# Kernel tuning notes

Hardware: AMD Instinct MI355X
Metric: run time of the kernel (lower is better)

Reference implementation:

```python
import jax, jax.numpy as jnp
import numpy as np

B, S, D, H, E, K = 4, 2048, 1024, 4096, 8, 2
CAP = 2048      # expert capacity (tokens)
ALPHA = 0.01    # load-balance loss coefficient


def setup_inputs() -> dict:
    key = jax.random.key(0)
    ks = jax.random.split(key, 8)
    def w(k, shape, fan_in):
        return jax.random.normal(k, shape, jnp.float32) * (fan_in ** -0.5)
    return {
        "input": jax.random.normal(ks[0], (B, S, D), jnp.float32),
        "rw": w(ks[1], (D, E), D), "rb": jnp.zeros((E,), jnp.float32),
        "w1": w(ks[2], (E, D, H), D), "b1": jnp.zeros((E, H), jnp.float32),
        "w2": w(ks[3], (E, H, D), H), "b2": jnp.zeros((E, D), jnp.float32),
        "ow1": w(ks[4], (D, H), D), "ob1": jnp.zeros((H,), jnp.float32),
        "ow2": w(ks[5], (H, D), H), "ob2": jnp.zeros((D,), jnp.float32),
    }


def _moe(x, rw, rb, w1, b1, w2, b2, ow1, ob1, ow2, ob2):
    Bx, Sx, Dx = x.shape
    N = Bx * Sx
    xf = x.reshape(N, Dx)

    # --- router: softmax -> top-k -> renormalize ---
    scores = jax.nn.softmax(xf @ rw + rb, axis=-1)          # [N,E]
    tw, ti = jax.lax.top_k(scores, K)                       # [N,K]
    tw = tw / tw.sum(-1, keepdims=True)
    onehot = jax.nn.one_hot(ti, E, dtype=xf.dtype)          # [N,K,E]
    w_ne = jnp.einsum('nk,nke->ne', tw, onehot)             # combine weight per (token, expert)
    mask = onehot.sum(1) > 0                                # [N,E]
    mi = mask.astype(jnp.int32)

    # exclusive rank of each token within its expert's queue (token order, as torch nonzero())
    rank = jnp.cumsum(mi, axis=0) - mi                      # [N,E]
    within = mask & (rank < CAP)
    over = mask & (rank >= CAP)

    # --- dispatch within-capacity tokens into [E, CAP] slots (sentinel = N) ---
    tok = jnp.broadcast_to(jnp.arange(N, dtype=jnp.int32)[:, None], (N, E))
    eid = jnp.broadcast_to(jnp.arange(E, dtype=jnp.int32)[None, :], (N, E))
    slot = jnp.where(within, rank, CAP)                     # non-assigned -> pad column
    buf = jnp.full((E, CAP + 1), N, dtype=jnp.int32)
    buf = buf.at[eid.reshape(-1), slot.reshape(-1)].set(tok.reshape(-1))
    buf = buf[:, :CAP]                                      # [E,CAP]

    xpad = jnp.concatenate([xf, jnp.zeros((1, Dx), xf.dtype)], axis=0)
    xd = xpad[buf]                                          # [E,CAP,D]

    # --- grouped expert FFN (Linear -> relu -> Linear) ---
    h = jax.nn.relu(jnp.einsum('ecd,edh->ech', xd, w1) + b1[:, None, :])
    y = jnp.einsum('ech,ehd->ecd', h, w2) + b2[:, None, :]  # [E,CAP,D]

    # combine weights gathered per slot; pad slots get weight 0
    wpad = jnp.concatenate([w_ne, jnp.zeros((1, E), w_ne.dtype)], axis=0)
    wc = wpad[buf, jnp.arange(E, dtype=jnp.int32)[:, None]]  # [E,CAP]

    outpad = jnp.zeros((N + 1, Dx), xf.dtype)
    outpad = outpad.at[buf.reshape(-1)].add((wc[..., None] * y).reshape(-1, Dx))
    out = outpad[:N]

    # --- overflow tokens -> shared overflow FFN (computed densely, masked by weight) ---
    w_of = (w_ne * over.astype(w_ne.dtype)).sum(-1)          # [N]
    yo = jax.nn.relu(xf @ ow1 + ob1) @ ow2 + ob2             # [N,D]
    out = out + w_of[:, None] * yo

    # --- aux load-balance loss (detached in torch via .item()) ---
    num = mi.sum(0)                                          # [E]
    cnt = jnp.minimum(num, CAP)
    f = cnt.astype(xf.dtype) / N
    p = (w_ne * within.astype(w_ne.dtype)).sum(0) / jnp.maximum(cnt, 1).astype(xf.dtype)
    aux = ALPHA * E * jnp.sum(f * p)
    return out.reshape(Bx, Sx, Dx), jax.lax.stop_gradient(aux)


def reference(input, rw, rb, w1, b1, w2, b2, ow1, ob1, ow2, ob2):
    return _moe(input, rw, rb, w1, b1, w2, b2, ow1, ob1, ow2, ob2)
```

## Files before the change

kernel.cpp:

```cpp
#include <hip/hip_runtime.h>
#include <cstdint>

typedef __attribute__((ext_vector_type(8))) short bf16x8;
typedef __attribute__((ext_vector_type(4))) float f32x4;

#define N_TOK    8192
#define DMODEL   1024
#define HDIM     4096
#define CAPACITY 2048

__device__ __forceinline__ unsigned short f2bf(float f) {
  unsigned u = __float_as_uint(f);
  u += 0x7FFFu + ((u >> 16) & 1u);
  return (unsigned short)(u >> 16);
}

__device__ __forceinline__ void gl_lds16(const unsigned short* g, unsigned short* l) {
  __builtin_amdgcn_global_load_lds(
      (const __attribute__((address_space(1))) void*)g,
      (__attribute__((address_space(3))) void*)l, 16, 0, 0);
}

__global__ void cvtx_kernel(const float* __restrict__ x, unsigned short* __restrict__ xb) {
  long i0 = ((long)blockIdx.x * 256 + threadIdx.x) * 16;
#pragma unroll
  for (int ii = 0; ii < 4; ii++) {
    float4 v = *(const float4*)(x + i0 + ii * 4);
    ushort4 u;
    u.x = f2bf(v.x); u.y = f2bf(v.y); u.z = f2bf(v.z); u.w = f2bf(v.w);
    *(ushort4*)(xb + i0 + ii * 4) = u;
  }
}

__global__ void router_kernel(const float* __restrict__ x, const float* __restrict__ rw,
                              const float* __restrict__ rb, int4* __restrict__ recs) {
  int wave = threadIdx.x >> 6;
  int lane = threadIdx.x & 63;
  int tok = blockIdx.x * 4 + wave;
  const float* xr = x + (long)tok * DMODEL;
  float s[8];
#pragma unroll
  for (int e = 0; e < 8; e++) s[e] = 0.f;
  for (int ii = 0; ii < DMODEL / 64; ii++) {
    int k = lane + 64 * ii;
    float xv = xr[k];
    const float* wr = rw + k * 8;
    float4 a = *(const float4*)wr;
    float4 b = *(const float4*)(wr + 4);
    s[0] += xv * a.x; s[1] += xv * a.y; s[2] += xv * a.z; s[3] += xv * a.w;
    s[4] += xv * b.x; s[5] += xv * b.y; s[6] += xv * b.z; s[7] += xv * b.w;
  }
#pragma unroll
  for (int m = 1; m < 64; m <<= 1) {
#pragma unroll
    for (int e = 0; e < 8; e++) s[e] += __shfl_xor(s[e], m);
  }
  if (lane == 0) {
#pragma unroll
    for (int e = 0; e < 8; e++) s[e] += rb[e];
    int b0 = 0; float v0 = s[0];
#pragma unroll
    for (int e = 1; e < 8; e++) if (s[e] > v0) { v0 = s[e]; b0 = e; }
    int b1 = -1; float v1 = 0.f;
#pragma unroll
    for (int e = 0; e < 8; e++) {
      if (e == b0) continue;
      if (b1 < 0 || s[e] > v1) { v1 = s[e]; b1 = e; }
    }
    float t0 = 1.f / (1.f + expf(v1 - v0));
    float t1 = 1.f - t0;
    recs[tok] = make_int4(b0, b1, __float_as_int(t0), __float_as_int(t1));
  }
}

__device__ __forceinline__ int bump16(uint4& v, int e) {
  unsigned sh = (e & 1) ? 16u : 0u;
  unsigned inc = 1u << sh;
  unsigned old;
  switch (e >> 1) {
    case 0: old = v.x; v.x += inc; break;
    case 1: old = v.y; v.y += inc; break;
    case 2: old = v.z; v.z += inc; break;
    default: old = v.w; v.w += inc; break;
  }
  return (int)((old >> sh) & 0xFFFFu);
}

__device__ __forceinline__ unsigned field16(uint4 v, int e) {
  unsigned w;
  switch (e >> 1) { case 0: w = v.x; break; case 1: w = v.y; break; case 2: w = v.z; break; default: w = v.w; break; }
  return (w >> ((e & 1) ? 16 : 0)) & 0xFFFFu;
}

__global__ void assign_kernel(const int4* __restrict__ recs, int* __restrict__ buf,
                              float* __restrict__ wc, int* __restrict__ cnt,
                              float* __restrict__ auxOut) {
  __shared__ uint4 sc[1024];
  __shared__ unsigned sco[1024];
  __shared__ float pnum[8];
  int tid = threadIdx.x;
  if (tid < 8) pnum[tid] = 0.f;
  int4 rc[8];
#pragma unroll
  for (int i = 0; i < 8; i++) {
    rc[i] = recs[tid * 8 + i];
    rc[i].x &= 7; rc[i].y &= 7;
  }
  uint4 c; c.x = c.y = c.z = c.w = 0u;
#pragma unroll
  for (int i = 0; i < 8; i++) { bump16(c, rc[i].x); bump16(c, rc[i].y); }
  sc[tid] = c;
  __syncthreads();
  for (int off = 1; off < 1024; off <<= 1) {
    uint4 v; v.x = v.y = v.z = v.w = 0u;
    if (tid >= off) v = sc[tid - off];
    __syncthreads();
    sc[tid].x += v.x; sc[tid].y += v.y; sc[tid].z += v.z; sc[tid].w += v.w;
    __syncthreads();
  }
  uint4 base; base.x = base.y = base.z = base.w = 0u;
  if (tid > 0) base = sc[tid - 1];
  uint4 totals = sc[1023];

  uint4 run = base;
  float wof[8];
  unsigned oc = 0;
#pragma unroll
  for (int i = 0; i < 8; i++) {
    int tk = tid * 8 + i;
    int e0 = rc[i].x, e1 = rc[i].y;
    float w0 = __int_as_float(rc[i].z);
    float w1 = __int_as_float(rc[i].w);
    float w = 0.f;
    int r0 = bump16(run, e0);
    if (r0 < CAPACITY) {
      buf[e0 * CAPACITY + r0] = tk;
      wc[e0 * CAPACITY + r0] = w0;
      atomicAdd(&pnum[e0], w0);
    } else w += w0;
    int r1 = bump16(run, e1);
    if (r1 < CAPACITY) {
      buf[e1 * CAPACITY + r1] = tk;
      wc[e1 * CAPACITY + r1] = w1;
      atomicAdd(&pnum[e1], w1);
    } else w += w1;
    wof[i] = w;
    if (w > 0.f) oc++;
  }
  sco[tid] = oc;
  __syncthreads();
  for (int off = 1; off < 1024; off <<= 1) {
    unsigned v = (tid >= off) ? sco[tid - off] : 0u;
    __syncthreads();
    sco[tid] += v;
    __syncthreads();
  }
  unsigned ob = (tid > 0) ? sco[tid - 1] : 0u;
  unsigned Ot = sco[1023];
#pragma unroll
  for (int i = 0; i < 8; i++) {
    if (wof[i] > 0.f) {
      unsigned slot = ob++;
      int ve = 8 + (int)(slot >> 11);
      buf[ve * CAPACITY + (int)(slot & 2047)] = tid * 8 + i;
      wc[ve * CAPACITY + (int)(slot & 2047)] = wof[i];
    }
  }
  __syncthreads();
  if (tid == 0) {
    float aux = 0.f;
#pragma unroll
    for (int e = 0; e < 8; e++) {
      int tot = (int)field16(totals, e);
      int c2 = tot < CAPACITY ? tot : CAPACITY;
      cnt[e] = c2;
      float f = (float)c2 / (float)N_TOK;
      float p = pnum[e] / (float)(c2 > 1 ? c2 : 1);
      aux += f * p;
    }
#pragma unroll
    for (int i = 0; i < 4; i++) {
      int c2 = (int)Ot - i * CAPACITY;
      c2 = c2 < 0 ? 0 : (c2 > CAPACITY ? CAPACITY : c2);
      cnt[8 + i] = c2;
    }
    auxOut[0] = 0.01f * 8.f * aux;
  }
}

__global__ __launch_bounds__(256) void transpose_all(
    const float* __restrict__ w1, const float* __restrict__ w2,
    const float* __restrict__ ow1, const float* __restrict__ ow2,
    unsigned short* __restrict__ wt1, unsigned short* __restrict__ wt2,
    long slotStride, int pairBase) {
  int pair = pairBase + blockIdx.x / 2048;
  int t = blockIdx.x & 2047;
  long srcOff = (long)pair * DMODEL * HDIM;
  long dstOff = (long)(blockIdx.x / 2048) * slotStride;
  const float* in; unsigned short* out; int R, C;
  if (t < 1024) {
    in = (pair < 8) ? w1 + srcOff : ow1;
    out = wt1 + dstOff;
    R = DMODEL; C = HDIM;
  } else {
    in = (pair < 8) ? w2 + srcOff : ow2;
    out = wt2 + dstOff;
    R = HDIM; C = DMODEL;
    t -= 1024;
  }
  int tr = t / (C >> 6);
  int tc = t % (C >> 6);
  int r0 = tr << 6, c0 = tc << 6;
  __shared__ float tl[64][65];
  int row = threadIdx.x >> 4, cg = threadIdx.x & 15;
#pragma unroll
  for (int i = 0; i < 4; i++) {
    int r = row + 16 * i;
    float4 v = *(const float4*)(in + (long)(r0 + r) * C + c0 + cg * 4);
    tl[r][cg * 4 + 0] = v.x; tl[r][cg * 4 + 1] = v.y;
    tl[r][cg * 4 + 2] = v.z; tl[r][cg * 4 + 3] = v.w;
  }
  __syncthreads();
#pragma unroll
  for (int i = 0; i < 4; i++) {
    int oc = row + 16 * i;
    ushort4 o;
    o.x = f2bf(tl[cg * 4 + 0][oc]);
    o.y = f2bf(tl[cg * 4 + 1][oc]);
    o.z = f2bf(tl[cg * 4 + 2][oc]);
    o.w = f2bf(tl[cg * 4 + 3][oc]);
    *(ushort4*)(out + (long)(c0 + oc) * R + r0 + cg * 4) = o;
  }
}


#define STAGE_PAIR(Abuf, Bbuf, kk)                                  \
  do {                                                              \
    _Pragma("unroll") for (int s = 0; s < 4; s++) {                 \
      gl_lds16(asrc[s] + (kk), &(Abuf)[wave * 2048 + s * 512]);     \
      gl_lds16(bsrc[s] + (kk), &(Bbuf)[wave * 2048 + s * 512]);     \
    }                                                               \
  } while (0)

__global__ __launch_bounds__(512, 2) void gemm1_kernel(
    const unsigned short* __restrict__ xb, const int* __restrict__ buf,
    const int* __restrict__ cnt, const unsigned short* __restrict__ wt1, long wtStride,
    const float* __restrict__ b1, const float* __restrict__ ob1,
    unsigned short* __restrict__ h, long hStride, int eBase,
    const unsigned short* __restrict__ zp) {
  int q = gridDim.x >> 3;
  int bx = blockIdx.x;
  int id = (bx & 7) * q + (bx >> 3);
  int e = eBase + id / 128;
  int rem = id % 128;
  int mb = rem >> 4, nb = rem & 15;
  int m0 = mb * 256, n0 = nb * 256;
  if (m0 >= cnt[e]) return;
  const int* bufe = buf + e * CAPACITY;
  int slot = e < 8 ? e : 8;
  const unsigned short* wte = wt1 + (long)slot * wtStride;
  const float* bias = (e < 8) ? b1 + (long)e * HDIM : ob1;
  unsigned short* he = h + (long)e * hStride;

  __shared__ unsigned short As[2][256 * 64];
  __shared__ unsigned short Bs[2][256 * 64];

  int tid = threadIdx.x;
  int wave = tid >> 6, lane = tid & 63;
  int l15 = lane & 15, hi = lane >> 4;
  int wr = wave >> 2, wc = wave & 3;
  int mo = wr * 128, no = wc * 64;

  int rlo = lane >> 3;
  int cg = (lane & 7) ^ rlo;
  const unsigned short* asrc[4];
  const unsigned short* bsrc[4];
#pragma unroll
  for (int s = 0; s < 4; s++) {
    int r = wave * 32 + s * 8 + rlo;
    int tok = bufe[m0 + r];
    asrc[s] = ((unsigned)tok < (unsigned)N_TOK) ? (xb + (long)tok * DMODEL + cg * 8)
                                                : (zp + cg * 8);
    bsrc[s] = wte + (long)(n0 + r) * DMODEL + cg * 8;
  }

  f32x4 zero4 = {0.f, 0.f, 0.f, 0.f};
  f32x4 acc[8][4];
#pragma unroll
  for (int mi = 0; mi < 8; mi++)
#pragma unroll
    for (int ni = 0; ni < 4; ni++) acc[mi][ni] = zero4;

  const int NT = DMODEL / 64;
  STAGE_PAIR(As[0], Bs[0], 0);
  __syncthreads();
  int cur = 0;
  for (int t = 0; t < NT; t++) {
    if (t + 1 < NT) {
      if (cur) STAGE_PAIR(As[0], Bs[0], (t + 1) * 64);
      else     STAGE_PAIR(As[1], Bs[1], (t + 1) * 64);
    }
    const unsigned short* Ac = As[cur];
    const unsigned short* Bc = Bs[cur];
#pragma unroll
    for (int ks = 0; ks < 2; ks++) {
      bf16x8 af[8], bfv[4];
#pragma unroll
      for (int mi = 0; mi < 8; mi++) {
        int r = mo + mi * 16 + l15;
        af[mi] = *(bf16x8*)&Ac[r * 64 + (((ks * 4 + hi) ^ (r & 7)) << 3)];
      }
#pragma unroll
      for (int ni = 0; ni < 4; ni++) {
        int r = no + ni * 16 + l15;
        bfv[ni] = *(bf16x8*)&Bc[r * 64 + (((ks * 4 + hi) ^ (r & 7)) << 3)];
      }
#pragma unroll
      for (int mi = 0; mi < 8; mi++)
#pragma unroll
        for (int ni = 0; ni < 4; ni++)
          acc[mi][ni] = __builtin_amdgcn_mfma_f32_16x16x32_bf16(af[mi], bfv[ni], acc[mi][ni], 0, 0, 0);
    }
    __syncthreads();
    cur ^= 1;
  }
#pragma unroll
  for (int ni = 0; ni < 4; ni++) {
    int col = n0 + no + ni * 16 + l15;
    float bv = bias[col];
#pragma unroll
    for (int mi = 0; mi < 8; mi++) {
#pragma unroll
      for (int j = 0; j < 4; j++) {
        int mr = m0 + mo + mi * 16 + hi * 4 + j;
        float val = acc[mi][ni][j] + bv;
        val = val > 0.f ? val : 0.f;
        he[(long)mr * HDIM + col] = f2bf(val);
      }
    }
  }
}

__global__ __launch_bounds__(512, 2) void gemm2_kernel(
    const unsigned short* __restrict__ h, long hStride,
    const unsigned short* __restrict__ wt2, long wtStride,
    const float* __restrict__ b2, const float* __restrict__ ob2,
    const int* __restrict__ buf, const float* __restrict__ wc,
    const int* __restrict__ cnt, float* __restrict__ out,
    int eBase, int per, int klen) {
  int q = gridDim.x >> 3;
  int bx = blockIdx.x;
  int id = (bx & 7) * q + (bx >> 3);
  int e = eBase + id / per;
  int rem = id % per;
  int tile = rem & 31;
  int kc = rem >> 5;
  int mb = tile >> 2, nb = tile & 3;
  int m0 = mb * 256, n0 = nb * 256;
  if (m0 >= cnt[e]) return;
  const int* bufe = buf + e * CAPACITY;
  const float* wce = wc + e * CAPACITY;
  int slot = e < 8 ? e : 8;
  const unsigned short* wte = wt2 + (long)slot * wtStride;
  const float* bias = (e < 8) ? b2 + (long)e * DMODEL : ob2;
  const unsigned short* he = h + (long)e * hStride;
  int kbase = kc * klen;

  __shared__ unsigned short As[2][256 * 64];
  __shared__ unsigned short Bs[2][256 * 64];

  int tid = threadIdx.x;
  int wave = tid >> 6, lane = tid & 63;
  int l15 = lane & 15, hi = lane >> 4;
  int wr = wave >> 2, wc2 = wave & 3;
  int mo = wr * 128, no = wc2 * 64;

  int rlo = lane >> 3;
  int cg = (lane & 7) ^ rlo;
  const unsigned short* asrc[4];
  const unsigned short* bsrc[4];
#pragma unroll
  for (int s = 0; s < 4; s++) {
    int r = wave * 32 + s * 8 + rlo;
    asrc[s] = he + (long)(m0 + r) * HDIM + kbase + cg * 8;
    bsrc[s] = wte + (long)(n0 + r) * HDIM + kbase + cg * 8;
  }

  f32x4 zero4 = {0.f, 0.f, 0.f, 0.f};
  f32x4 acc[8][4];
#pragma unroll
  for (int mi = 0; mi < 8; mi++)
#pragma unroll
    for (int ni = 0; ni < 4; ni++) acc[mi][ni] = zero4;

  const int NT = klen / 64;
  STAGE_PAIR(As[0], Bs[0], 0);
  __syncthreads();
  int cur = 0;
  for (int t = 0; t < NT; t++) {
    if (t + 1 < NT) {
      if (cur) STAGE_PAIR(As[0], Bs[0], (t + 1) * 64);
      else     STAGE_PAIR(As[1], Bs[1], (t + 1) * 64);
    }
    const unsigned short* Ac = As[cur];
    const unsigned short* Bc = Bs[cur];
#pragma unroll
    for (int ks = 0; ks < 2; ks++) {
      bf16x8 af[8], bfv[4];
#pragma unroll
      for (int mi = 0; mi < 8; mi++) {
        int r = mo + mi * 16 + l15;
        af[mi] = *(bf16x8*)&Ac[r * 64 + (((ks * 4 + hi) ^ (r & 7)) << 3)];
      }
#pragma unroll
      for (int ni = 0; ni < 4; ni++) {
        int r = no + ni * 16 + l15;
        bfv[ni] = *(bf16x8*)&Bc[r * 64 + (((ks * 4 + hi) ^ (r & 7)) << 3)];
      }
#pragma unroll
      for (int mi = 0; mi < 8; mi++)
#pragma unroll
        for (int ni = 0; ni < 4; ni++)
          acc[mi][ni] = __builtin_amdgcn_mfma_f32_16x16x32_bf16(af[mi], bfv[ni], acc[mi][ni], 0, 0, 0);
    }
    __syncthreads();
    cur ^= 1;
  }
  float bcol[4];
#pragma unroll
  for (int ni = 0; ni < 4; ni++)
    bcol[ni] = (kc == 0) ? bias[n0 + no + ni * 16 + l15] : 0.f;
#pragma unroll
  for (int mi = 0; mi < 8; mi++) {
#pragma unroll
    for (int j = 0; j < 4; j++) {
      int m = m0 + mo + mi * 16 + hi * 4 + j;
      int t = bufe[m];
      if ((unsigned)t >= (unsigned)N_TOK) continue;
      float wv = wce[m];
      float* orow = out + (long)t * DMODEL;
#pragma unroll
      for (int ni = 0; ni < 4; ni++) {
        int col = n0 + no + ni * 16 + l15;
        float val = wv * (acc[mi][ni][j] + bcol[ni]);
        atomicAdd(orow + col, val);
      }
    }
  }
}

extern "C" void kernel_launch(void* const* d_in, const int* in_sizes, int n_in,
                              void* d_out, int out_size, void* d_ws, size_t ws_size,
                              hipStream_t stream) {
  const float* x   = (const float*)d_in[0];
  const float* rw  = (const float*)d_in[1];
  const float* rb  = (const float*)d_in[2];
  const float* w1  = (const float*)d_in[3];
  const float* b1  = (const float*)d_in[4];
  const float* w2  = (const float*)d_in[5];
  const float* b2  = (const float*)d_in[6];
  const float* ow1 = (const float*)d_in[7];
  const float* ob1 = (const float*)d_in[8];
  const float* ow2 = (const float*)d_in[9];
  const float* ob2 = (const float*)d_in[10];
  float* out = (float*)d_out;

  const long WSLOT = (long)DMODEL * HDIM;
  const long HSLOT = (long)CAPACITY * HDIM;

  bool fused = ws_size >= 380ull * 1024 * 1024;

  char* ws = (char*)d_ws;
  int4* recs = (int4*)(ws);
  int*  buf  = (int*)(ws + 131072);
  float* wcp = (float*)(ws + 229376);
  int*  cnt  = (int*)(ws + 327680);
  unsigned short* zp = (unsigned short*)(ws + 331776);
  unsigned short* xb  = (unsigned short*)(ws + 1048576);
  unsigned short* wt1 = (unsigned short*)(ws + 17825792);
  unsigned short* wt2;
  unsigned short* h;
  if (fused) {
    wt2 = (unsigned short*)(ws + 93323264);
    h   = (unsigned short*)(ws + 168820736);
  } else {
    wt2 = (unsigned short*)(ws + 26214400);
    h   = (unsigned short*)(ws + 34603008);
  }

  hipMemsetAsync(d_out, 0, (size_t)out_size * sizeof(float), stream);
  hipMemsetAsync(buf, 0xFF, 12 * CAPACITY * sizeof(int), stream);
  hipMemsetAsync(wcp, 0, 12 * CAPACITY * sizeof(float), stream);
  hipMemsetAsync(zp, 0, 2048, stream);

  cvtx_kernel<<<2048, 256, 0, stream>>>(x, xb);
  router_kernel<<<2048, 256, 0, stream>>>(x, rw, rb, recs);
  assign_kernel<<<1, 1024, 0, stream>>>(recs, buf, wcp, cnt, out + (long)N_TOK * DMODEL);

  if (fused) {
    transpose_all<<<9 * 2048, 256, 0, stream>>>(w1, w2, ow1, ow2, wt1, wt2, WSLOT, 0);
    gemm1_kernel<<<12 * 128, 512, 0, stream>>>(xb, buf, cnt, wt1, WSLOT, b1, ob1, h, HSLOT, 0, zp);
    gemm2_kernel<<<12 * 64, 512, 0, stream>>>(h, HSLOT, wt2, WSLOT, b2, ob2, buf, wcp, cnt, out,
                                              0, 64, HDIM / 2);
  } else {
    for (int e = 0; e < 12; e++) {
      if (e <= 8)
        transpose_all<<<2048, 256, 0, stream>>>(w1, w2, ow1, ow2, wt1, wt2, 0, e);
      gemm1_kernel<<<128, 512, 0, stream>>>(xb, buf, cnt, wt1, 0, b1, ob1, h, 0, e, zp);
      gemm2_kernel<<<64, 512, 0, stream>>>(h, 0, wt2, 0, b2, ob2, buf, wcp, cnt, out,
                                           e, 64, HDIM / 2);
    }
  }
}
```

Baseline: 654.1 us.

## Restructure GEMM K-loop with two-deep prefetch, explicit vmcnt waits and MFMA priority

Both expert GEMM kernels replace the compiler-scheduled double-buffer loop with a manual pipeline. It issues two stages of global-to-LDS loads up front, waits with s_waitcnt vmcnt(8) so one stage stays in flight, and uses raw s_barrier with sched_barrier fences instead of __syncthreads. The MFMA block is also wrapped in s_setprio to favour math issue. The aim is to hide global load latency behind compute, at the cost of relying on an exact count of outstanding vector memory ops (8 per stage), which breaks if the staging code changes.

```diff
diff --git a/kernel.cpp b/kernel.cpp
--- a/kernel.cpp
+++ b/kernel.cpp
@@ -20,6 +20,14 @@
       (const __attribute__((address_space(1))) void*)g,
       (__attribute__((address_space(3))) void*)l, 16, 0, 0);
 }
+
+#define WAITV8() do { asm volatile("s_waitcnt vmcnt(8)" ::: "memory"); \
+                      __builtin_amdgcn_sched_barrier(0); } while (0)
+#define WAITV0() do { asm volatile("s_waitcnt vmcnt(0)" ::: "memory"); \
+                      __builtin_amdgcn_sched_barrier(0); } while (0)
+#define BAR()    do { __builtin_amdgcn_sched_barrier(0);               \
+                      __builtin_amdgcn_s_barrier();                    \
+                      __builtin_amdgcn_sched_barrier(0); } while (0)
 
 __global__ void cvtx_kernel(const float* __restrict__ x, unsigned short* __restrict__ xb) {
   long i0 = ((long)blockIdx.x * 256 + threadIdx.x) * 16;
@@ -242,6 +250,41 @@
     }                                                               \
   } while (0)
 
+#define COMPUTE_TILE(Ac, Bc)                                                   \
+  _Pragma("unroll") for (int ks = 0; ks < 2; ks++) {                           \
+    bf16x8 af[8], bfv[4];                                                      \
+    _Pragma("unroll") for (int mi = 0; mi < 8; mi++) {                         \
+      int r = mo + mi * 16 + l15;                                              \
+      af[mi] = *(bf16x8*)&(Ac)[r * 64 + (((ks * 4 + hi) ^ (r & 7)) << 3)];     \
+    }                                                                          \
+    _Pragma("unroll") for (int ni = 0; ni < 4; ni++) {                         \
+      int r = no + ni * 16 + l15;                                              \
+      bfv[ni] = *(bf16x8*)&(Bc)[r * 64 + (((ks * 4 + hi) ^ (r & 7)) << 3)];    \
+    }                                                                          \
+    __builtin_amdgcn_s_setprio(1);                                             \
+    _Pragma("unroll") for (int mi = 0; mi < 8; mi++)                           \
+      _Pragma("unroll") for (int ni = 0; ni < 4; ni++)                         \
+        acc[mi][ni] = __builtin_amdgcn_mfma_f32_16x16x32_bf16(af[mi], bfv[ni], acc[mi][ni], 0, 0, 0); \
+    __builtin_amdgcn_s_setprio(0);                                             \
+  }
+
+#define K_PIPELINE(NT)                                              \
+  do {                                                              \
+    STAGE_PAIR(As[0], Bs[0], 0);                                    \
+    STAGE_PAIR(As[1], Bs[1], 64);                                   \
+    for (int t = 0; t < (NT); t++) {                                \
+      if (t + 1 < (NT)) { WAITV8(); } else { WAITV0(); }            \
+      BAR();                                                        \
+      if (t & 1) { COMPUTE_TILE(As[1], Bs[1]); }                    \
+      else       { COMPUTE_TILE(As[0], Bs[0]); }                    \
+      BAR();                                                        \
+      if (t + 2 < (NT)) {                                           \
+        if (t & 1) STAGE_PAIR(As[1], Bs[1], (t + 2) * 64);          \
+        else       STAGE_PAIR(As[0], Bs[0], (t + 2) * 64);          \
+      }                                                             \
+    }                                                               \
+  } while (0)
+
 __global__ __launch_bounds__(512, 2) void gemm1_kernel(
     const unsigned short* __restrict__ xb, const int* __restrict__ buf,
     const int* __restrict__ cnt, const unsigned short* __restrict__ wt1, long wtStride,
@@ -268,8 +311,8 @@
   int tid = threadIdx.x;
   int wave = tid >> 6, lane = tid & 63;
   int l15 = lane & 15, hi = lane >> 4;
-  int wr = wave >> 2, wc = wave & 3;
-  int mo = wr * 128, no = wc * 64;
+  int wr = wave >> 2, wcv = wave & 3;
+  int mo = wr * 128, no = wcv * 64;
 
   int rlo = lane >> 3;
   int cg = (lane & 7) ^ rlo;
@@ -291,39 +334,8 @@
 #pragma unroll
     for (int ni = 0; ni < 4; ni++) acc[mi][ni] = zero4;
 
-  const int NT = DMODEL / 64;
-  STAGE_PAIR(As[0], Bs[0], 0);
-  __syncthreads();
-  int cur = 0;
-  for (int t = 0; t < NT; t++) {
-    if (t + 1 < NT) {
-      if (cur) STAGE_PAIR(As[0], Bs[0], (t + 1) * 64);
-      else     STAGE_PAIR(As[1], Bs[1], (t + 1) * 64);
-    }
-    const unsigned short* Ac = As[cur];
-    const unsigned short* Bc = Bs[cur];
-#pragma unroll
-    for (int ks = 0; ks < 2; ks++) {
-      bf16x8 af[8], bfv[4];
-#pragma unroll
-      for (int mi = 0; mi < 8; mi++) {
-        int r = mo + mi * 16 + l15;
-        af[mi] = *(bf16x8*)&Ac[r * 64 + (((ks * 4 + hi) ^ (r & 7)) << 3)];
-      }
-#pragma unroll
-      for (int ni = 0; ni < 4; ni++) {
-        int r = no + ni * 16 + l15;
-        bfv[ni] = *(bf16x8*)&Bc[r * 64 + (((ks * 4 + hi) ^ (r & 7)) << 3)];
-      }
-#pragma unroll
-      for (int mi = 0; mi < 8; mi++)
-#pragma unroll
-        for (int ni = 0; ni < 4; ni++)
-          acc[mi][ni] = __builtin_amdgcn_mfma_f32_16x16x32_bf16(af[mi], bfv[ni], acc[mi][ni], 0, 0, 0);
-    }
-    __syncthreads();
-    cur ^= 1;
-  }
+  K_PIPELINE(DMODEL / 64);
+
 #pragma unroll
   for (int ni = 0; ni < 4; ni++) {
     int col = n0 + no + ni * 16 + l15;
@@ -372,8 +384,8 @@
   int tid = threadIdx.x;
   int wave = tid >> 6, lane = tid & 63;
   int l15 = lane & 15, hi = lane >> 4;
-  int wr = wave >> 2, wc2 = wave & 3;
-  int mo = wr * 128, no = wc2 * 64;
+  int wr = wave >> 2, wcv = wave & 3;
+  int mo = wr * 128, no = wcv * 64;
 
   int rlo = lane >> 3;
   int cg = (lane & 7) ^ rlo;
@@ -393,39 +405,8 @@
 #pragma unroll
     for (int ni = 0; ni < 4; ni++) acc[mi][ni] = zero4;
 
-  const int NT = klen / 64;
-  STAGE_PAIR(As[0], Bs[0], 0);
-  __syncthreads();
-  int cur = 0;
-  for (int t = 0; t < NT; t++) {
-    if (t + 1 < NT) {
-      if (cur) STAGE_PAIR(As[0], Bs[0], (t + 1) * 64);
-      else     STAGE_PAIR(As[1], Bs[1], (t + 1) * 64);
-    }
-    const unsigned short* Ac = As[cur];
-    const unsigned short* Bc = Bs[cur];
-#pragma unroll
-    for (int ks = 0; ks < 2; ks++) {
-      bf16x8 af[8], bfv[4];
-#pragma unroll
-      for (int mi = 0; mi < 8; mi++) {
-        int r = mo + mi * 16 + l15;
-        af[mi] = *(bf16x8*)&Ac[r * 64 + (((ks * 4 + hi) ^ (r & 7)) << 3)];
-      }
-#pragma unroll
-      for (int ni = 0; ni < 4; ni++) {
-        int r = no + ni * 16 + l15;
-        bfv[ni] = *(bf16x8*)&Bc[r * 64 + (((ks * 4 + hi) ^ (r & 7)) << 3)];
-      }
-#pragma unroll
-      for (int mi = 0; mi < 8; mi++)
-#pragma unroll
-        for (int ni = 0; ni < 4; ni++)
-          acc[mi][ni] = __builtin_amdgcn_mfma_f32_16x16x32_bf16(af[mi], bfv[ni], acc[mi][ni], 0, 0, 0);
-    }
-    __syncthreads();
-    cur ^= 1;
-  }
+  K_PIPELINE(klen / 64);
+
   float bcol[4];
 #pragma unroll
   for (int ni = 0; ni < 4; ni++)
```

Result: slower. 2.269 ms (median of 4 runs) (+246.9%).
